# Performance work log

Measured on AMD Instinct MI355X. Metric: run time of the kernel, lower is better.

## Reference

```python
import jax, jax.numpy as jnp
import numpy as np

NUM_HEADS = 16
D_MODEL = 1024
DEPTH = D_MODEL // NUM_HEADS
THRESHOLD = 0.1
BATCH = 2
SEQ = 2048


def setup_inputs() -> dict:
    key = jax.random.key(0)
    ks = jax.random.split(key, 9)
    w_scale = 1.0 / np.sqrt(D_MODEL)
    Q = jax.random.normal(ks[0], (BATCH, SEQ, D_MODEL), dtype=jnp.float32)
    T = jax.random.normal(ks[1], (BATCH, SEQ, D_MODEL), dtype=jnp.float32)
    V = jax.random.normal(ks[2], (BATCH, SEQ, D_MODEL), dtype=jnp.float32)
    Wq = jax.random.normal(ks[3], (NUM_HEADS, D_MODEL, DEPTH), dtype=jnp.float32) * w_scale
    Wk = jax.random.normal(ks[4], (NUM_HEADS, D_MODEL, DEPTH), dtype=jnp.float32) * w_scale
    Wv = jax.random.normal(ks[5], (NUM_HEADS, D_MODEL, DEPTH), dtype=jnp.float32) * w_scale
    Wo = jax.random.normal(ks[6], (D_MODEL, D_MODEL), dtype=jnp.float32) * w_scale
    bq = jnp.zeros((NUM_HEADS, DEPTH), dtype=jnp.float32)
    bk = jnp.zeros((NUM_HEADS, DEPTH), dtype=jnp.float32)
    bv = jnp.zeros((NUM_HEADS, DEPTH), dtype=jnp.float32)
    bo = jnp.zeros((D_MODEL,), dtype=jnp.float32)
    return {"Q": Q, "T": T, "V": V, "Wq": Wq, "bq": bq, "Wk": Wk, "bk": bk,
            "Wv": Wv, "bv": bv, "Wo": Wo, "bo": bo}


def reference(Q, T, V, Wq, bq, Wk, bk, Wv, bv, Wo, bo):
    # Per-head projections (stacked over heads): [B,S,D] x [H,D,E] -> [B,H,S,E]
    q = jnp.einsum('bsd,hde->bhse', Q, Wq) + bq[None, :, None, :]
    k = jnp.einsum('bsd,hde->bhse', T, Wk) + bk[None, :, None, :]
    v = jnp.einsum('bsd,hde->bhse', V, Wv) + bv[None, :, None, :]

    # Raw scores (NOT pre-scaled): [B,H,S,S]
    scores = jnp.einsum('bhqe,bhke->bhqk', q, k)
    # tf.where(A>thr, A, -2**32 * cast(A>thr)) -> failing entries become 0
    scores = jnp.where(scores > THRESHOLD, scores, jnp.zeros((), scores.dtype))
    # M = 1 - lower_band(ones): +1 on strictly upper-triangular entries
    seq = scores.shape[-1]
    upper = jnp.triu(jnp.ones((seq, seq), dtype=scores.dtype), k=1)
    scores = (scores + upper) / jnp.sqrt(jnp.asarray(DEPTH, scores.dtype))

    attn = jax.nn.softmax(scores, axis=-1)
    out = jnp.einsum('bhqk,bhke->bhqe', attn, v)  # [B,H,S,E]
    B, H, S, E = out.shape
    concat = out.transpose(0, 2, 1, 3).reshape(B, S, H * E)  # [B,S,D]
    return concat @ Wo + bo
```

## Files before the change

### kernel.cpp

```cpp
#include <hip/hip_runtime.h>
#include <stdint.h>


typedef __attribute__((ext_vector_type(8))) short bf16x8;
typedef __attribute__((ext_vector_type(4))) float f32x4;

#define DEVFN static __device__ __forceinline__

static constexpr int S_ = 2048;
static constexpr int H_ = 16;

DEVFN unsigned short f2bf(float x) {
  union { float f; uint32_t u; } v; v.f = x;
  const uint32_t r = v.u + 0x7fffu + ((v.u >> 16) & 1u);
  return (unsigned short)(r >> 16);
}

DEVFN f32x4 fzero() { f32x4 v = {0.f, 0.f, 0.f, 0.f}; return v; }

DEVFN void gld_lds16(const void* g, void* lds) {
  __builtin_amdgcn_global_load_lds(
      (const __attribute__((address_space(1))) void*)g,
      (__attribute__((address_space(3))) void*)lds, 16, 0, 0);
}

__global__ void prep_weights(const float* __restrict__ Wq, const float* __restrict__ Wk,
                             const float* __restrict__ Wv, const float* __restrict__ Wo,
                             unsigned short* __restrict__ dstBase) {
  const int z = blockIdx.z;
  const float* src = (z == 0) ? Wq : (z == 1) ? Wk : (z == 2) ? Wv : Wo;
  unsigned short* dst = dstBase + (size_t)z * (1024u * 1024u);
  const int idx = blockIdx.x * 256 + threadIdx.x;
  const int c = idx & 1023;
  const int d0 = (idx >> 10) << 3;
  unsigned short hv[8];
#pragma unroll
  for (int t = 0; t < 8; ++t) {
    const int d = d0 + t;
    const float v = (z < 3) ? src[(size_t)((c >> 6) * 1024 + d) * 64 + (c & 63)]
                            : src[(size_t)d * 1024 + c];
    hv[t] = f2bf(v);
  }
  *(uint4*)(dst + (size_t)c * 1024 + d0) = *(const uint4*)hv;
}

__global__ __launch_bounds__(256, 2)
void proj_gemm(const float* __restrict__ Qm, const float* __restrict__ Tm,
               const float* __restrict__ Vm, const unsigned short* __restrict__ Wt,
               const float* __restrict__ bq, const float* __restrict__ bk,
               const float* __restrict__ bv, unsigned short* __restrict__ qb,
               unsigned short* __restrict__ kb, unsigned short* __restrict__ vtb) {
  __shared__ unsigned short At[128 * 32];
  __shared__ unsigned short Bt[128 * 32];

  const int tid = threadIdx.x;
  const int lane = tid & 63;
  const int w = tid >> 6;
  const int g = lane >> 4, c = lane & 15;
  const int wm = w >> 1, wn = w & 1;

  const int m0 = blockIdx.x * 128;
  const int proj = blockIdx.y >> 3;
  const int n0 = (blockIdx.y & 7) * 128;

  const float* Asrc = (proj == 0) ? Qm : (proj == 1) ? Tm : Vm;
  const unsigned short* W = Wt + (size_t)proj * (1024u * 1024u);

  f32x4 acc[4][4];
#pragma unroll
  for (int i = 0; i < 4; ++i)
#pragma unroll
    for (int j = 0; j < 4; ++j) acc[i][j] = fzero();

  const int ar = tid >> 1;
  const int ah = tid & 1;

  for (int kt = 0; kt < 32; ++kt) {
    const int k0 = kt * 32;
    {
      const float* s = Asrc + (size_t)(m0 + ar) * 1024 + k0 + ah * 16;
      const float4 f0 = ((const float4*)s)[0];
      const float4 f1 = ((const float4*)s)[1];
      const float4 f2 = ((const float4*)s)[2];
      const float4 f3 = ((const float4*)s)[3];
      unsigned short hv[16];
      hv[0] = f2bf(f0.x); hv[1] = f2bf(f0.y); hv[2] = f2bf(f0.z); hv[3] = f2bf(f0.w);
      hv[4] = f2bf(f1.x); hv[5] = f2bf(f1.y); hv[6] = f2bf(f1.z); hv[7] = f2bf(f1.w);
      hv[8] = f2bf(f2.x); hv[9] = f2bf(f2.y); hv[10] = f2bf(f2.z); hv[11] = f2bf(f2.w);
      hv[12] = f2bf(f3.x); hv[13] = f2bf(f3.y); hv[14] = f2bf(f3.z); hv[15] = f2bf(f3.w);
      const int swz = (ar >> 1) & 3;
      *(uint4*)&At[ar * 32 + ((ah * 2 + 0) ^ swz) * 8] = *(const uint4*)&hv[0];
      *(uint4*)&At[ar * 32 + ((ah * 2 + 1) ^ swz) * 8] = *(const uint4*)&hv[8];
    }
#pragma unroll
    for (int u = 0; u < 2; ++u) {
      const int row = w * 32 + u * 16 + (lane >> 2);
      const int ch = (lane & 3) ^ ((row >> 1) & 3);
      gld_lds16(W + (size_t)(n0 + row) * 1024 + k0 + ch * 8,
                &Bt[(w * 32 + u * 16) * 32]);
    }
    __syncthreads();

    bf16x8 af[4], bfr[4];
#pragma unroll
    for (int mi = 0; mi < 4; ++mi) {
      const int row = wm * 64 + mi * 16 + c;
      af[mi] = *(const bf16x8*)&At[row * 32 + ((g ^ ((row >> 1) & 3))) * 8];
    }
#pragma unroll
    for (int ni = 0; ni < 4; ++ni) {
      const int row = wn * 64 + ni * 16 + c;
      bfr[ni] = *(const bf16x8*)&Bt[row * 32 + ((g ^ ((row >> 1) & 3))) * 8];
    }
#pragma unroll
    for (int mi = 0; mi < 4; ++mi)
#pragma unroll
      for (int ni = 0; ni < 4; ++ni)
        acc[mi][ni] = __builtin_amdgcn_mfma_f32_16x16x32_bf16(af[mi], bfr[ni],
                                                              acc[mi][ni], 0, 0, 0);
    __syncthreads();
  }

  const float* bias = (proj == 0) ? bq : (proj == 1) ? bk : bv;
#pragma unroll
  for (int ni = 0; ni < 4; ++ni) {
    const int colb = n0 + wn * 64 + ni * 16 + c;
    const float bc = bias[colb];
    const int hh = colb >> 6, e = colb & 63;
#pragma unroll
    for (int mi = 0; mi < 4; ++mi) {
#pragma unroll
      for (int r = 0; r < 4; ++r) {
        const int row = m0 + wm * 64 + mi * 16 + g * 4 + r;
        const int bb = row >> 11, s = row & 2047;
        const float val = acc[mi][ni][r] + bc;
        if (proj < 2) {
          unsigned short* d = (proj == 0) ? qb : kb;
          d[(((size_t)(bb * H_ + hh)) * S_ + s) * 64 + e] = f2bf(val);
        } else {
          vtb[(((size_t)(bb * H_ + hh)) * 64 + e) * S_ + s] = f2bf(val);
        }
      }
    }
  }
}

__global__ __launch_bounds__(256, 4)
void attn_kernel(const unsigned short* __restrict__ qb,
                 const unsigned short* __restrict__ kb,
                 const unsigned short* __restrict__ vtb,
                 unsigned short* __restrict__ att) {
  __shared__ unsigned short Kt[2][64 * 64];
  __shared__ unsigned short Vt[2][64 * 64];
  __shared__ unsigned short Pt[4][16 * 64];

  const int tid = threadIdx.x;
  const int lane = tid & 63;
  const int w = tid >> 6;
  const int g = lane >> 4, c = lane & 15;

  const int orig = blockIdx.x;
  const int logical = ((orig & 7) << 7) | (orig >> 3);
  const int qblk = logical & 31;
  const int bh = logical >> 5;
  const int hh = bh & 15, bz = bh >> 4;

  const int q0w = qblk * 64 + w * 16;
  const unsigned short* qh = qb + (size_t)bh * S_ * 64;
  const unsigned short* kh = kb + (size_t)bh * S_ * 64;
  const unsigned short* vh = vtb + (size_t)bh * 64 * S_;

  bf16x8 aq[2];
#pragma unroll
  for (int t = 0; t < 2; ++t)
    aq[t] = *(const bf16x8*)&qh[(size_t)(q0w + c) * 64 + t * 32 + g * 8];

  f32x4 O[4];
#pragma unroll
  for (int ne = 0; ne < 4; ++ne) O[ne] = fzero();
  float l_lane = 0.f;

  constexpr float L2E = 1.4426950408889634f;
  const float S2 = 0.125f * L2E;
  const float B2 = 0.125f * L2E;
  const int iq = q0w + c;

  const int srow = w * 8 + (lane >> 3);
  const int sch = lane & 7;

  {
#pragma unroll
    for (int u = 0; u < 2; ++u) {
      const int row = u * 32 + srow;
      gld_lds16(kh + (size_t)row * 64 + (sch ^ (row & 7)) * 8,
                &Kt[0][(u * 32 + w * 8) * 64]);
      gld_lds16(vh + (size_t)row * S_ + (sch ^ (row & 7)) * 8,
                &Vt[0][(u * 32 + w * 8) * 64]);
    }
  }
  __syncthreads();

  for (int jt = 0; jt < 32; ++jt) {
    const int cur = jt & 1;
    const int j0 = jt * 64;

    if (jt < 31) {
      const int jn = j0 + 64;
#pragma unroll
      for (int u = 0; u < 2; ++u) {
        const int row = u * 32 + srow;
        gld_lds16(kh + (size_t)(jn + row) * 64 + (sch ^ (row & 7)) * 8,
                  &Kt[cur ^ 1][(u * 32 + w * 8) * 64]);
        gld_lds16(vh + (size_t)row * S_ + jn + (sch ^ (row & 7)) * 8,
                  &Vt[cur ^ 1][(u * 32 + w * 8) * 64]);
      }
    }

    f32x4 sa[4];
#pragma unroll
    for (int mi = 0; mi < 4; ++mi) sa[mi] = fzero();
#pragma unroll
    for (int ks = 0; ks < 2; ++ks) {
#pragma unroll
      for (int mi = 0; mi < 4; ++mi) {
        const int row = mi * 16 + c;
        const bf16x8 ka =
            *(const bf16x8*)&Kt[cur][row * 64 + ((ks * 4 + g) ^ (row & 7)) * 8];
        sa[mi] = __builtin_amdgcn_mfma_f32_16x16x32_bf16(ka, aq[ks], sa[mi], 0, 0, 0);
      }
    }

    float pe[16];
    const bool allUp = (j0 >= q0w + 16);
    const bool noneUp = (j0 + 63 <= q0w);
    if (allUp || noneUp) {
      const float bb = allUp ? B2 : 0.f;
#pragma unroll
      for (int i = 0; i < 16; ++i) {
        const float v = sa[i >> 2][i & 3];
        const float arg = (v > 0.1f) ? __builtin_fmaf(v, S2, bb) : bb;
        pe[i] = __builtin_amdgcn_exp2f(arg);
      }
    } else {
#pragma unroll
      for (int mi = 0; mi < 4; ++mi)
#pragma unroll
        for (int r = 0; r < 4; ++r) {
          const float v = sa[mi][r];
          const float bb = (j0 + mi * 16 + g * 4 + r > iq) ? B2 : 0.f;
          const float arg = (v > 0.1f) ? __builtin_fmaf(v, S2, bb) : bb;
          pe[mi * 4 + r] = __builtin_amdgcn_exp2f(arg);
        }
    }

    {
      float s01 = pe[0] + pe[1], s23 = pe[2] + pe[3];
      float s45 = pe[4] + pe[5], s67 = pe[6] + pe[7];
      float s89 = pe[8] + pe[9], sab = pe[10] + pe[11];
      float scd = pe[12] + pe[13], sef = pe[14] + pe[15];
      l_lane += ((s01 + s23) + (s45 + s67)) + ((s89 + sab) + (scd + sef));
    }

#pragma unroll
    for (int mi = 0; mi < 4; ++mi) {
      uint2 d;
      asm("v_cvt_pk_bf16_f32 %0, %1, %2"
          : "=v"(d.x) : "v"(pe[mi * 4 + 0]), "v"(pe[mi * 4 + 1]));
      asm("v_cvt_pk_bf16_f32 %0, %1, %2"
          : "=v"(d.y) : "v"(pe[mi * 4 + 2]), "v"(pe[mi * 4 + 3]));
      const int pc = (2 * mi + (g >> 1)) ^ (c & 7);
      *(uint2*)&Pt[w][c * 64 + pc * 8 + (g & 1) * 4] = d;
    }
    asm volatile("s_waitcnt lgkmcnt(0)" ::: "memory");
    __builtin_amdgcn_sched_barrier(0);

#pragma unroll
    for (int ks = 0; ks < 2; ++ks) {
      const bf16x8 pa =
          *(const bf16x8*)&Pt[w][c * 64 + (((ks * 4 + g) ^ (c & 7))) * 8];
#pragma unroll
      for (int ne = 0; ne < 4; ++ne) {
        const int e = ne * 16 + c;
        const bf16x8 bv8 =
            *(const bf16x8*)&Vt[cur][e * 64 + ((ks * 4 + g) ^ (e & 7)) * 8];
        O[ne] = __builtin_amdgcn_mfma_f32_16x16x32_bf16(pa, bv8, O[ne], 0, 0, 0);
      }
    }
    __syncthreads();
  }

  float l = l_lane;
  l += __shfl_xor(l, 16);
  l += __shfl_xor(l, 32);
  const float invl = 1.f / l;
  const int base = (lane >> 2) & 12;
  float il[4];
#pragma unroll
  for (int r = 0; r < 4; ++r) il[r] = __shfl(invl, base + r);
#pragma unroll
  for (int r = 0; r < 4; ++r) {
    const int qg = q0w + g * 4 + r;
    const size_t ro = ((size_t)(bz * S_ + qg)) * 1024 + hh * 64;
#pragma unroll
    for (int ne = 0; ne < 4; ++ne)
      att[ro + ne * 16 + c] = f2bf(O[ne][r] * il[r]);
  }
}

__global__ __launch_bounds__(256, 2)
void out_gemm(const unsigned short* __restrict__ att,
              const unsigned short* __restrict__ WoT,
              const float* __restrict__ bo, float* __restrict__ outp) {
  __shared__ unsigned short At[128 * 32];
  __shared__ unsigned short Bt[128 * 32];

  const int tid = threadIdx.x;
  const int lane = tid & 63;
  const int w = tid >> 6;
  const int g = lane >> 4, c = lane & 15;
  const int wm = w >> 1, wn = w & 1;
  const int m0 = blockIdx.x * 128;
  const int n0 = blockIdx.y * 128;

  f32x4 acc[4][4];
#pragma unroll
  for (int i = 0; i < 4; ++i)
#pragma unroll
    for (int j = 0; j < 4; ++j) acc[i][j] = fzero();

  for (int kt = 0; kt < 32; ++kt) {
    const int k0 = kt * 32;
#pragma unroll
    for (int u = 0; u < 2; ++u) {
      const int row = w * 32 + u * 16 + (lane >> 2);
      const int ch = (lane & 3) ^ ((row >> 1) & 3);
      gld_lds16(att + (size_t)(m0 + row) * 1024 + k0 + ch * 8,
                &At[(w * 32 + u * 16) * 32]);
      gld_lds16(WoT + (size_t)(n0 + row) * 1024 + k0 + ch * 8,
                &Bt[(w * 32 + u * 16) * 32]);
    }
    __syncthreads();

    bf16x8 af[4], bfr[4];
#pragma unroll
    for (int mi = 0; mi < 4; ++mi) {
      const int row = wm * 64 + mi * 16 + c;
      af[mi] = *(const bf16x8*)&At[row * 32 + ((g ^ ((row >> 1) & 3))) * 8];
    }
#pragma unroll
    for (int ni = 0; ni < 4; ++ni) {
      const int row = wn * 64 + ni * 16 + c;
      bfr[ni] = *(const bf16x8*)&Bt[row * 32 + ((g ^ ((row >> 1) & 3))) * 8];
    }
#pragma unroll
    for (int mi = 0; mi < 4; ++mi)
#pragma unroll
      for (int ni = 0; ni < 4; ++ni)
        acc[mi][ni] = __builtin_amdgcn_mfma_f32_16x16x32_bf16(af[mi], bfr[ni],
                                                              acc[mi][ni], 0, 0, 0);
    __syncthreads();
  }

#pragma unroll
  for (int ni = 0; ni < 4; ++ni) {
    const int colb = n0 + wn * 64 + ni * 16 + c;
    const float bc = bo[colb];
#pragma unroll
    for (int mi = 0; mi < 4; ++mi)
#pragma unroll
      for (int r = 0; r < 4; ++r) {
        const int row = m0 + wm * 64 + mi * 16 + g * 4 + r;
        outp[(size_t)row * 1024 + colb] = acc[mi][ni][r] + bc;
      }
  }
}

extern "C" void kernel_launch(void* const* d_in, const int* in_sizes, int n_in,
                              void* d_out, int out_size, void* d_ws, size_t ws_size,
                              hipStream_t stream) {
  const float* Q  = (const float*)d_in[0];
  const float* T  = (const float*)d_in[1];
  const float* V  = (const float*)d_in[2];
  const float* Wq = (const float*)d_in[3];
  const float* bq = (const float*)d_in[4];
  const float* Wk = (const float*)d_in[5];
  const float* bk = (const float*)d_in[6];
  const float* Wv = (const float*)d_in[7];
  const float* bv = (const float*)d_in[8];
  const float* Wo = (const float*)d_in[9];
  const float* bo = (const float*)d_in[10];

  const size_t MB = 1024ull * 1024ull;
  if (ws_size < 40 * MB) return;

  uint8_t* ws = (uint8_t*)d_ws;
  unsigned short* Wt  = (unsigned short*)(ws);
  unsigned short* qb  = (unsigned short*)(ws + 8 * MB);
  unsigned short* kb  = (unsigned short*)(ws + 16 * MB);
  unsigned short* vtb = (unsigned short*)(ws + 24 * MB);
  unsigned short* attb = (unsigned short*)(ws + 32 * MB);

  prep_weights<<<dim3(512, 1, 4), 256, 0, stream>>>(Wq, Wk, Wv, Wo, Wt);
  proj_gemm<<<dim3(32, 24), 256, 0, stream>>>(Q, T, V, Wt, bq, bk, bv, qb, kb, vtb);
  attn_kernel<<<dim3(1024), 256, 0, stream>>>(qb, kb, vtb, attb);
  out_gemm<<<dim3(32, 8), 256, 0, stream>>>(attb, Wt + 3ull * 1024ull * 1024ull,
                                            bo, (float*)d_out);
}
```

Baseline: 142.7 us.

## Double-buffer LDS tiles in projection and output GEMMs, add MFMA priority hints

Both GEMM kernels now prefetch the next K tile into a second LDS buffer while computing the current one, removing one barrier per iteration. The projection kernel converts fp32 to bf16 with packed hardware conversion instructions instead of manual rounding. Launch bounds rise to 3 blocks per CU, and the attention kernel raises wave priority around its MFMA sections. Doubling LDS use and tightening register limits may cause spills or cap occupancy.

```diff
diff --git a/kernel.cpp b/kernel.cpp
--- a/kernel.cpp
+++ b/kernel.cpp
@@ -44,14 +44,14 @@
   *(uint4*)(dst + (size_t)c * 1024 + d0) = *(const uint4*)hv;
 }
 
-__global__ __launch_bounds__(256, 2)
+__global__ __launch_bounds__(256, 3)
 void proj_gemm(const float* __restrict__ Qm, const float* __restrict__ Tm,
                const float* __restrict__ Vm, const unsigned short* __restrict__ Wt,
                const float* __restrict__ bq, const float* __restrict__ bk,
                const float* __restrict__ bv, unsigned short* __restrict__ qb,
                unsigned short* __restrict__ kb, unsigned short* __restrict__ vtb) {
-  __shared__ unsigned short At[128 * 32];
-  __shared__ unsigned short Bt[128 * 32];
+  __shared__ unsigned short At[2][128 * 32];
+  __shared__ unsigned short Bt[2][128 * 32];
 
   const int tid = threadIdx.x;
   const int lane = tid & 63;
@@ -74,43 +74,56 @@
 
   const int ar = tid >> 1;
   const int ah = tid & 1;
+  const int swzA = (ar >> 1) & 3;
+  const float* aBase = Asrc + (size_t)(m0 + ar) * 1024 + ah * 16;
+  const int brow0 = w * 32 + (lane >> 2);
+  const int bch = lane & 3;
+
+  auto stage = [&](int kt, int buf) {
+#pragma unroll
+    for (int u = 0; u < 2; ++u) {
+      const int row = brow0 + u * 16;
+      const int ch = bch ^ ((row >> 1) & 3);
+      gld_lds16(W + (size_t)(n0 + row) * 1024 + kt * 32 + ch * 8,
+                &Bt[buf][(w * 32 + u * 16) * 32]);
+    }
+    const float* s = aBase + kt * 32;
+    const float4 f0 = ((const float4*)s)[0];
+    const float4 f1 = ((const float4*)s)[1];
+    const float4 f2 = ((const float4*)s)[2];
+    const float4 f3 = ((const float4*)s)[3];
+    uint32_t d0, d1, d2, d3, d4, d5, d6, d7;
+    asm("v_cvt_pk_bf16_f32 %0, %1, %2" : "=v"(d0) : "v"(f0.x), "v"(f0.y));
+    asm("v_cvt_pk_bf16_f32 %0, %1, %2" : "=v"(d1) : "v"(f0.z), "v"(f0.w));
+    asm("v_cvt_pk_bf16_f32 %0, %1, %2" : "=v"(d2) : "v"(f1.x), "v"(f1.y));
+    asm("v_cvt_pk_bf16_f32 %0, %1, %2" : "=v"(d3) : "v"(f1.z), "v"(f1.w));
+    asm("v_cvt_pk_bf16_f32 %0, %1, %2" : "=v"(d4) : "v"(f2.x), "v"(f2.y));
+    asm("v_cvt_pk_bf16_f32 %0, %1, %2" : "=v"(d5) : "v"(f2.z), "v"(f2.w));
+    asm("v_cvt_pk_bf16_f32 %0, %1, %2" : "=v"(d6) : "v"(f3.x), "v"(f3.y));
+    asm("v_cvt_pk_bf16_f32 %0, %1, %2" : "=v"(d7) : "v"(f3.z), "v"(f3.w));
+    uint4 lo; lo.x = d0; lo.y = d1; lo.z = d2; lo.w = d3;
+    uint4 hi; hi.x = d4; hi.y = d5; hi.z = d6; hi.w = d7;
+    *(uint4*)&At[buf][ar * 32 + ((ah * 2 + 0) ^ swzA) * 8] = lo;
+    *(uint4*)&At[buf][ar * 32 + ((ah * 2 + 1) ^ swzA) * 8] = hi;
+  };
+
+  stage(0, 0);
+  __syncthreads();
 
   for (int kt = 0; kt < 32; ++kt) {
-    const int k0 = kt * 32;
-    {
-      const float* s = Asrc + (size_t)(m0 + ar) * 1024 + k0 + ah * 16;
-      const float4 f0 = ((const float4*)s)[0];
-      const float4 f1 = ((const float4*)s)[1];
-      const float4 f2 = ((const float4*)s)[2];
-      const float4 f3 = ((const float4*)s)[3];
-      unsigned short hv[16];
-      hv[0] = f2bf(f0.x); hv[1] = f2bf(f0.y); hv[2] = f2bf(f0.z); hv[3] = f2bf(f0.w);
-      hv[4] = f2bf(f1.x); hv[5] = f2bf(f1.y); hv[6] = f2bf(f1.z); hv[7] = f2bf(f1.w);
-      hv[8] = f2bf(f2.x); hv[9] = f2bf(f2.y); hv[10] = f2bf(f2.z); hv[11] = f2bf(f2.w);
-      hv[12] = f2bf(f3.x); hv[13] = f2bf(f3.y); hv[14] = f2bf(f3.z); hv[15] = f2bf(f3.w);
-      const int swz = (ar >> 1) & 3;
-      *(uint4*)&At[ar * 32 + ((ah * 2 + 0) ^ swz) * 8] = *(const uint4*)&hv[0];
-      *(uint4*)&At[ar * 32 + ((ah * 2 + 1) ^ swz) * 8] = *(const uint4*)&hv[8];
-    }
-#pragma unroll
-    for (int u = 0; u < 2; ++u) {
-      const int row = w * 32 + u * 16 + (lane >> 2);
-      const int ch = (lane & 3) ^ ((row >> 1) & 3);
-      gld_lds16(W + (size_t)(n0 + row) * 1024 + k0 + ch * 8,
-                &Bt[(w * 32 + u * 16) * 32]);
-    }
-    __syncthreads();
+    const int buf = kt & 1;
+    if (kt < 31) stage(kt + 1, buf ^ 1);
 
     bf16x8 af[4], bfr[4];
 #pragma unroll
     for (int mi = 0; mi < 4; ++mi) {
       const int row = wm * 64 + mi * 16 + c;
-      af[mi] = *(const bf16x8*)&At[row * 32 + ((g ^ ((row >> 1) & 3))) * 8];
+      af[mi] = *(const bf16x8*)&At[buf][row * 32 + ((g ^ ((row >> 1) & 3))) * 8];
     }
 #pragma unroll
     for (int ni = 0; ni < 4; ++ni) {
       const int row = wn * 64 + ni * 16 + c;
-      bfr[ni] = *(const bf16x8*)&Bt[row * 32 + ((g ^ ((row >> 1) & 3))) * 8];
+      bfr[ni] = *(const bf16x8*)&Bt[buf][row * 32 + ((g ^ ((row >> 1) & 3))) * 8];
     }
 #pragma unroll
     for (int mi = 0; mi < 4; ++mi)
@@ -219,6 +232,7 @@
     f32x4 sa[4];
 #pragma unroll
     for (int mi = 0; mi < 4; ++mi) sa[mi] = fzero();
+    __builtin_amdgcn_s_setprio(1);
 #pragma unroll
     for (int ks = 0; ks < 2; ++ks) {
 #pragma unroll
@@ -229,6 +243,7 @@
         sa[mi] = __builtin_amdgcn_mfma_f32_16x16x32_bf16(ka, aq[ks], sa[mi], 0, 0, 0);
       }
     }
+    __builtin_amdgcn_s_setprio(0);
 
     float pe[16];
     const bool allUp = (j0 >= q0w + 16);
@@ -274,6 +289,7 @@
     asm volatile("s_waitcnt lgkmcnt(0)" ::: "memory");
     __builtin_amdgcn_sched_barrier(0);
 
+    __builtin_amdgcn_s_setprio(1);
 #pragma unroll
     for (int ks = 0; ks < 2; ++ks) {
       const bf16x8 pa =
@@ -286,6 +302,7 @@
         O[ne] = __builtin_amdgcn_mfma_f32_16x16x32_bf16(pa, bv8, O[ne], 0, 0, 0);
       }
     }
+    __builtin_amdgcn_s_setprio(0);
     __syncthreads();
   }
 
@@ -307,12 +324,12 @@
   }
 }
 
-__global__ __launch_bounds__(256, 2)
+__global__ __launch_bounds__(256, 3)
 void out_gemm(const unsigned short* __restrict__ att,
               const unsigned short* __restrict__ WoT,
               const float* __restrict__ bo, float* __restrict__ outp) {
-  __shared__ unsigned short At[128 * 32];
-  __shared__ unsigned short Bt[128 * 32];
+  __shared__ unsigned short At[2][128 * 32];
+  __shared__ unsigned short Bt[2][128 * 32];
 
   const int tid = threadIdx.x;
   const int lane = tid & 63;
@@ -328,29 +345,38 @@
 #pragma unroll
     for (int j = 0; j < 4; ++j) acc[i][j] = fzero();
 
+  const int brow0 = w * 32 + (lane >> 2);
+  const int bch = lane & 3;
+
+  auto stage = [&](int kt, int buf) {
+#pragma unroll
+    for (int u = 0; u < 2; ++u) {
+      const int row = brow0 + u * 16;
+      const int ch = bch ^ ((row >> 1) & 3);
+      gld_lds16(att + (size_t)(m0 + row) * 1024 + kt * 32 + ch * 8,
+                &At[buf][(w * 32 + u * 16) * 32]);
+      gld_lds16(WoT + (size_t)(n0 + row) * 1024 + kt * 32 + ch * 8,
+                &Bt[buf][(w * 32 + u * 16) * 32]);
+    }
+  };
+
+  stage(0, 0);
+  __syncthreads();
+
   for (int kt = 0; kt < 32; ++kt) {
-    const int k0 = kt * 32;
-#pragma unroll
-    for (int u = 0; u < 2; ++u) {
-      const int row = w * 32 + u * 16 + (lane >> 2);
-      const int ch = (lane & 3) ^ ((row >> 1) & 3);
-      gld_lds16(att + (size_t)(m0 + row) * 1024 + k0 + ch * 8,
-                &At[(w * 32 + u * 16) * 32]);
-      gld_lds16(WoT + (size_t)(n0 + row) * 1024 + k0 + ch * 8,
-                &Bt[(w * 32 + u * 16) * 32]);
-    }
-    __syncthreads();
+    const int buf = kt & 1;
+    if (kt < 31) stage(kt + 1, buf ^ 1);
 
     bf16x8 af[4], bfr[4];
 #pragma unroll
     for (int mi = 0; mi < 4; ++mi) {
       const int row = wm * 64 + mi * 16 + c;
-      af[mi] = *(const bf16x8*)&At[row * 32 + ((g ^ ((row >> 1) & 3))) * 8];
+      af[mi] = *(const bf16x8*)&At[buf][row * 32 + ((g ^ ((row >> 1) & 3))) * 8];
     }
 #pragma unroll
     for (int ni = 0; ni < 4; ++ni) {
       const int row = wn * 64 + ni * 16 + c;
-      bfr[ni] = *(const bf16x8*)&Bt[row * 32 + ((g ^ ((row >> 1) & 3))) * 8];
+      bfr[ni] = *(const bf16x8*)&Bt[buf][row * 32 + ((g ^ ((row >> 1) & 3))) * 8];
     }
 #pragma unroll
     for (int mi = 0; mi < 4; ++mi)
```

After: 145.6 us. 2.1% more time.
